# Kernel optimization log

Hardware: AMD Instinct MI355X
Metric: run time of the kernel (lower is better)

The kernel has to match this reference:

```python
import jax, jax.numpy as jnp
import numpy as np

N, E = 50000, 800000
IN_F, OUT_F, H = 128, 128, 4
D = OUT_F // H  # head dim
NEG_SLOPE = 0.2
EPS = 1e-12


def setup_inputs() -> dict:
    key = jax.random.key(0)
    ks = jax.random.split(key, 10)
    s = 1.0 / np.sqrt(IN_F)
    return {
        "x": jax.random.normal(ks[0], (N, IN_F), jnp.float32),
        "W_src": jax.random.normal(ks[1], (IN_F, H * D), jnp.float32) * s,
        "b_src": jnp.zeros((H * D,), jnp.float32),
        "W_dst": jax.random.normal(ks[2], (IN_F, H * D), jnp.float32) * s,
        "b_dst": jnp.zeros((H * D,), jnp.float32),
        "attn": jax.random.normal(ks[3], (H, D), jnp.float32) * (1.0 / np.sqrt(D)),
        "out_bias": jnp.zeros((H * D,), jnp.float32),
        "ln_w": jnp.ones((OUT_F,), jnp.float32),
        "ln_b": jnp.zeros((OUT_F,), jnp.float32),
        "src": jax.random.randint(ks[4], (E,), 0, N, jnp.int32),
        "dst": jax.random.randint(ks[5], (E,), 0, N, jnp.int32),
    }


def reference(x, W_src, b_src, W_dst, b_dst, attn, out_bias, ln_w, ln_b, src, dst):
    n = x.shape[0]
    # GATv2Conv (share_weights=False): separate source/dest projections
    fs = (x @ W_src + b_src).reshape(n, H, D)  # [N,H,D]
    fd = (x @ W_dst + b_dst).reshape(n, H, D)
    # per-edge scores: e_ij = attn . leaky_relu(fs[u] + fd[v])
    e = jax.nn.leaky_relu(fs[src] + fd[dst], NEG_SLOPE)  # [E,H,D]
    logits = jnp.einsum("ehd,hd->eh", e, attn)  # [E,H]
    # edge softmax over incoming edges of each dst node
    m = jax.ops.segment_max(logits, dst, num_segments=n)  # [N,H]
    ex = jnp.exp(logits - m[dst])
    denom = jax.ops.segment_sum(ex, dst, num_segments=n)  # [N,H]
    alpha = ex / denom[dst]  # [E,H]
    # aggregate: sum_j alpha_ij * fs[j]
    msg = alpha[:, :, None] * fs[src]  # [E,H,D]
    rst = jax.ops.segment_sum(msg, dst, num_segments=n)  # [N,H,D]
    h = rst.reshape(n, H * D) + out_bias
    # LayerNorm (biased variance, eps inside sqrt)
    u = h.mean(-1, keepdims=True)
    s = jnp.mean((h - u) ** 2, -1, keepdims=True)
    h = (h - u) / jnp.sqrt(s + EPS)
    h = ln_w * h + ln_b
    # activation = elu; dropout p=0 -> identity
    return jax.nn.elu(h)
```

## Files before the change

kernel.cpp:

```cpp
#include <hip/hip_runtime.h>
#include <hip/hip_bf16.h>

constexpr int NF = 128;

using bf16x8 = __attribute__((ext_vector_type(8))) short;
using f32x4v = __attribute__((ext_vector_type(4))) float;

__device__ __forceinline__ unsigned short f2bs(float f) {
    return __builtin_bit_cast(unsigned short, __float2bfloat16(f));
}
__device__ __forceinline__ void unpack8(float4 raw, float* a) {
    unsigned u0 = __float_as_uint(raw.x);
    unsigned u1 = __float_as_uint(raw.y);
    unsigned u2 = __float_as_uint(raw.z);
    unsigned u3 = __float_as_uint(raw.w);
    a[0] = __uint_as_float(u0 << 16);
    a[1] = __uint_as_float(u0 & 0xffff0000u);
    a[2] = __uint_as_float(u1 << 16);
    a[3] = __uint_as_float(u1 & 0xffff0000u);
    a[4] = __uint_as_float(u2 << 16);
    a[5] = __uint_as_float(u2 & 0xffff0000u);
    a[6] = __uint_as_float(u3 << 16);
    a[7] = __uint_as_float(u3 & 0xffff0000u);
}

__global__ void GraphAttnLayer_70196945486348_kernel() {}

__device__ __forceinline__ void gemm_tile(
    const float* __restrict__ x,
    const unsigned short* __restrict__ Wb2,
    const float* __restrict__ bsrc, const float* __restrict__ bdst,
    unsigned short* __restrict__ fs, float* __restrict__ fd,
    int tile, int N)
{
    __shared__ float xs[32][129];
    const int t = threadIdx.x;
    const int lane = t & 63;
    const int wave = t >> 6;
    const int m_base = tile * 32;
    if (m_base >= N) return;
    const int lm = lane & 15;
    const int kq = (lane >> 4) * 8;

    bf16x8 bfrag[4][4];
    float bias[4];
#pragma unroll
    for (int c = 0; c < 4; ++c) {
        int col = wave * 64 + c * 16 + lm;
        bias[c] = (col < 128) ? bsrc[col] : bdst[col - 128];
#pragma unroll
        for (int s = 0; s < 4; ++s)
            bfrag[c][s] = *(const bf16x8*)(Wb2 + ((size_t)((c * 4 + s) * 256 + t)) * 8);
    }

#pragma unroll
    for (int q = 0; q < 4; ++q) {
        int idx = q * 256 + t;
        int row = idx >> 5;
        int c4  = (idx & 31) * 4;
        int grow = m_base + row;
        if (grow >= N) grow = N - 1;
        float4 v = *(const float4*)(x + (size_t)grow * NF + c4);
        xs[row][c4 + 0] = v.x;
        xs[row][c4 + 1] = v.y;
        xs[row][c4 + 2] = v.z;
        xs[row][c4 + 3] = v.w;
    }
    __syncthreads();

    for (int r = 0; r < 2; ++r) {
        int m0 = m_base + r * 16;
        if (m0 >= N) break;
        bf16x8 afrag[4];
#pragma unroll
        for (int s = 0; s < 4; ++s) {
            const float* xp = &xs[r * 16 + lm][s * 32 + kq];
#pragma unroll
            for (int j = 0; j < 8; ++j)
                afrag[s][j] = (short)f2bs(xp[j]);
        }
#pragma unroll
        for (int c = 0; c < 4; ++c) {
            f32x4v acc = {0.f, 0.f, 0.f, 0.f};
#pragma unroll
            for (int s = 0; s < 4; ++s)
                acc = __builtin_amdgcn_mfma_f32_16x16x32_bf16(afrag[s], bfrag[c][s], acc, 0, 0, 0);
            int col = wave * 64 + c * 16 + lm;
            int cc = col & 127;
#pragma unroll
            for (int rr = 0; rr < 4; ++rr) {
                int rowd = m0 + (lane >> 4) * 4 + rr;
                if (rowd < N) {
                    float v = acc[rr] + bias[c];
                    if (col < 128) fs[(size_t)rowd * NF + cc] = f2bs(v);
                    else           fd[(size_t)rowd * NF + cc] = v;
                }
            }
        }
    }
}

__global__ __launch_bounds__(256) void hist_prep_kernel(
    const int* __restrict__ dst,
    int* __restrict__ cntT,
    const float* __restrict__ Wsrc, const float* __restrict__ Wdst,
    unsigned short* __restrict__ Wb2,
    int* __restrict__ state,
    int E, int C, int B, int NSB)
{
    __shared__ int lh[256];
    const int t = threadIdx.x;
    int gi = blockIdx.x * 256 + t;
    if (gi < NSB) state[gi] = 0;
    if (gi < 16 * 256) {
        int j = gi >> 8;
        int tt = gi & 255;
        int wave = tt >> 6;
        int lane = tt & 63;
        int lm = lane & 15;
        int kq = (lane >> 4) * 8;
        int c = j >> 2, s = j & 3;
        int col = wave * 64 + c * 16 + lm;
        int ks = s * 32 + kq;
        bf16x8 frag;
#pragma unroll
        for (int m = 0; m < 8; ++m) {
            float v = (col < 128) ? Wsrc[(ks + m) * NF + col]
                                  : Wdst[(ks + m) * NF + (col - 128)];
            frag[m] = (short)f2bs(v);
        }
        *(bf16x8*)(Wb2 + (size_t)gi * 8) = frag;
    }

    lh[t] = 0;
    __syncthreads();
    int e0 = blockIdx.x * 4096;
#pragma unroll
    for (int j = 0; j < 16; ++j) {
        int e = e0 + j * 256 + t;
        if (e < E) atomicAdd(&lh[dst[e] >> 8], 1);
    }
    __syncthreads();
    if (t < B) cntT[t * C + blockIdx.x] = lh[t];
}

__global__ __launch_bounds__(256) void scan_kernel(
    const int* __restrict__ cntT, int* __restrict__ baseBC,
    int* __restrict__ state, int M)
{
    int b = blockIdx.x, t = threadIdx.x;
    int i = b * 256 + t;
    int v = (i < M) ? cntT[i] : 0;

    __shared__ int arr[256];
    __shared__ int s_bofs;
    arr[t] = v;
    __syncthreads();
    for (int off = 1; off < 256; off <<= 1) {
        int u = (t >= off) ? arr[t - off] : 0;
        __syncthreads();
        arr[t] += u;
        __syncthreads();
    }
    int total = arr[255];

    if (t < 64) {
        if (t == 0) {
            int word = ((b == 0 ? 2 : 1) << 30) | total;
            atomicExch(&state[b], word);
        }
        int bofs = 0;
        if (b > 0) {
            int base = b;
            for (;;) {
                int j = base - 1 - t;
                int sv = 0, f = 1;
                if (j >= 0) {
                    sv = __hip_atomic_load(&state[j], __ATOMIC_RELAXED,
                                           __HIP_MEMORY_SCOPE_AGENT);
                    f = ((unsigned)sv) >> 30;
                }
                unsigned long long notready = __ballot(f == 0);
                if (notready) continue;
                unsigned long long has2 = __ballot(f == 2);
                if (has2) {
                    int k = (int)(__ffsll((unsigned long long)has2) - 1);
                    int val = (t <= k) ? (sv & 0x3FFFFFFF) : 0;
#pragma unroll
                    for (int off = 32; off; off >>= 1) val += __shfl_xor(val, off);
                    bofs += val;
                    break;
                } else {
                    int val = (j >= 0) ? (sv & 0x3FFFFFFF) : 0;
#pragma unroll
                    for (int off = 32; off; off >>= 1) val += __shfl_xor(val, off);
                    bofs += val;
                    base -= 64;
                }
            }
            if (t == 0) atomicExch(&state[b], (2 << 30) | (bofs + total));
        }
        if (t == 0) s_bofs = bofs;
    }
    __syncthreads();
    int excl = arr[t] - v + s_bofs;
    if (i < M) baseBC[i] = excl;
}

__global__ __launch_bounds__(256) void scatter_gemm_kernel(
    const int* __restrict__ dst, const int* __restrict__ src,
    const int* __restrict__ baseBC, unsigned* __restrict__ pairs,
    const float* __restrict__ x, const unsigned short* __restrict__ Wb2,
    const float* __restrict__ bsrc, const float* __restrict__ bdst,
    unsigned short* __restrict__ fs, float* __restrict__ fd,
    int N, int E, int C, int B)
{
    __shared__ int base_lds[256];
    __shared__ int lcnt[256];
    int t = threadIdx.x;
    if (blockIdx.x < (unsigned)C) {
        int chunk = blockIdx.x;
        if (t < B) base_lds[t] = baseBC[t * C + chunk];
        lcnt[t] = 0;
        __syncthreads();
        int e0 = chunk * 4096;
#pragma unroll
        for (int j = 0; j < 16; ++j) {
            int e = e0 + j * 256 + t;
            if (e < E) {
                int d = dst[e];
                int b = d >> 8;
                int r = atomicAdd(&lcnt[b], 1);
                pairs[base_lds[b] + r] = ((unsigned)(d & 255) << 16) | (unsigned)src[e];
            }
        }
    } else {
        gemm_tile(x, Wb2, bsrc, bdst, fs, fd, blockIdx.x - C, N);
    }
}

__global__ __launch_bounds__(256) void sort_gemm_kernel(
    const unsigned* __restrict__ pairs, const int* __restrict__ baseBC,
    int* __restrict__ rowptr, unsigned short* __restrict__ src_sorted,
    const float* __restrict__ x, const unsigned short* __restrict__ Wb2,
    const float* __restrict__ bsrc, const float* __restrict__ bdst,
    unsigned short* __restrict__ fs, float* __restrict__ fd,
    int N, int E, int C, int B, int T1)
{
    __shared__ int h[256];
    __shared__ int arr[256];
    __shared__ int cur[256];
    __shared__ unsigned short sorted[16384];
    int t = threadIdx.x;
    if (blockIdx.x < (unsigned)B) {
        int b = blockIdx.x;
        int segbase = baseBC[b * C];
        int end = (b + 1 < B) ? baseBC[(b + 1) * C] : E;
        int count = end - segbase;

        h[t] = 0;
        __syncthreads();
        for (int i = t; i < count; i += 256)
            atomicAdd(&h[pairs[segbase + i] >> 16], 1);
        __syncthreads();
        int v = h[t];
        arr[t] = v;
        __syncthreads();
        for (int off = 1; off < 256; off <<= 1) {
            int u = (t >= off) ? arr[t - off] : 0;
            __syncthreads();
            arr[t] += u;
            __syncthreads();
        }
        int excl = arr[t] - v;
        int node = b * 256 + t;
        if (node <= N) rowptr[node] = segbase + excl;
        cur[t] = excl;
        __syncthreads();
        for (int i = t; i < count; i += 256) {
            unsigned p = pairs[segbase + i];
            int r = atomicAdd(&cur[p >> 16], 1);
            sorted[r] = (unsigned short)(p & 0xFFFF);
        }
        __syncthreads();
        for (int i = t; i < count; i += 256)
            src_sorted[segbase + i] = sorted[i];
    } else {
        gemm_tile(x, Wb2, bsrc, bdst, fs, fd, T1 + (blockIdx.x - B), N);
    }
}

__global__ __launch_bounds__(256) void node_kernel(
    const float4* __restrict__ fsq,
    const int* __restrict__ rowptr, const unsigned short* __restrict__ src_sorted,
    const float4* __restrict__ attn4,
    const float4* __restrict__ obias4,
    const float4* __restrict__ lnw4,
    const float4* __restrict__ lnb4,
    float4* __restrict__ out4, int N)
{
    int lane = threadIdx.x & 63;
    int es = lane >> 4;
    int g  = lane & 15;
    int n = blockIdx.x * 4 + (threadIdx.x >> 6);
    if (n >= N) return;

    float4 fda = out4[(size_t)n * 32 + g * 2];
    float4 fdb = out4[(size_t)n * 32 + g * 2 + 1];
    float4 ava = attn4[g * 2];
    float4 avb = attn4[g * 2 + 1];
    float fd[8] = {fda.x, fda.y, fda.z, fda.w, fdb.x, fdb.y, fdb.z, fdb.w};
    float av[8] = {ava.x, ava.y, ava.z, ava.w, avb.x, avb.y, avb.z, avb.w};

    int beg = rowptr[n], end = rowptr[n + 1];
    float l = 0.f;
    float ac[8] = {0.f, 0.f, 0.f, 0.f, 0.f, 0.f, 0.f, 0.f};

    for (int j = beg; j < end; j += 4) {
        int idx = j + es;
        bool valid = idx < end;
        int s = src_sorted[valid ? idx : (end - 1)];
        float4 raw = fsq[(size_t)s * 16 + g];
        float a[8];
        unpack8(raw, a);
        float p = 0.f;
#pragma unroll
        for (int d = 0; d < 8; ++d) {
            float t = a[d] + fd[d];
            t = fmaxf(t, 0.2f * t);
            p += av[d] * t;
        }
        p += __shfl_xor(p, 1);
        p += __shfl_xor(p, 2);
        float e = valid ? __expf(p) : 0.f;
        l += e;
#pragma unroll
        for (int d = 0; d < 8; ++d) ac[d] += e * a[d];
    }

    l += __shfl_xor(l, 16);
    l += __shfl_xor(l, 32);
#pragma unroll
    for (int d = 0; d < 8; ++d) {
        ac[d] += __shfl_xor(ac[d], 16);
        ac[d] += __shfl_xor(ac[d], 32);
    }

    float rl = (l > 0.f) ? (1.f / l) : 0.f;
    float4 oba = obias4[g * 2];
    float4 obb = obias4[g * 2 + 1];
    float ob[8] = {oba.x, oba.y, oba.z, oba.w, obb.x, obb.y, obb.z, obb.w};
    float h[8];
    float s1 = 0.f, s2 = 0.f;
#pragma unroll
    for (int d = 0; d < 8; ++d) {
        h[d] = ac[d] * rl + ob[d];
        s1 += h[d];
        s2 += h[d] * h[d];
    }
    s1 += __shfl_xor(s1, 1); s2 += __shfl_xor(s2, 1);
    s1 += __shfl_xor(s1, 2); s2 += __shfl_xor(s2, 2);
    s1 += __shfl_xor(s1, 4); s2 += __shfl_xor(s2, 4);
    s1 += __shfl_xor(s1, 8); s2 += __shfl_xor(s2, 8);

    float u = s1 * (1.f / NF);
    float var = s2 * (1.f / NF) - u * u;
    float rstd = rsqrtf(fmaxf(var, 0.f) + 1e-12f);
    float4 gwa = lnw4[g * 2], gwb = lnw4[g * 2 + 1];
    float4 gba = lnb4[g * 2], gbb = lnb4[g * 2 + 1];
    float gw[8] = {gwa.x, gwa.y, gwa.z, gwa.w, gwb.x, gwb.y, gwb.z, gwb.w};
    float gb[8] = {gba.x, gba.y, gba.z, gba.w, gbb.x, gbb.y, gbb.z, gbb.w};
    float z[8];
#pragma unroll
    for (int d = 0; d < 8; ++d) {
        float y = gw[d] * ((h[d] - u) * rstd) + gb[d];
        z[d] = (y > 0.f) ? y : (__expf(y) - 1.f);
    }
    if (es == 0) {
        out4[(size_t)n * 32 + g * 2]     = make_float4(z[0], z[1], z[2], z[3]);
        out4[(size_t)n * 32 + g * 2 + 1] = make_float4(z[4], z[5], z[6], z[7]);
    }
}

extern "C" void kernel_launch(void* const* d_in, const int* in_sizes, int n_in,
                              void* d_out, int out_size, void* d_ws, size_t ws_size,
                              hipStream_t stream)
{
    const float* x    = (const float*)d_in[0];
    const float* Wsrc = (const float*)d_in[1];
    const float* bsrc = (const float*)d_in[2];
    const float* Wdst = (const float*)d_in[3];
    const float* bdst = (const float*)d_in[4];
    const float4* attn4 = (const float4*)d_in[5];
    const float4* obias4= (const float4*)d_in[6];
    const float4* lnw4  = (const float4*)d_in[7];
    const float4* lnb4  = (const float4*)d_in[8];
    const int* src = (const int*)d_in[9];
    const int* dst = (const int*)d_in[10];
    int N = in_sizes[0] / NF;
    int E = in_sizes[9];

    int C = (E + 4095) / 4096;
    int B = (N + 255) / 256;
    int M = B * C;
    int NSB = (M + 255) / 256;
    int T = (N + 31) / 32;
    int T1 = T / 2;
    int T2 = T - T1;

    int* cntT = (int*)d_ws;
    int* baseBC = cntT + M;
    int* state = baseBC + M;
    int* rowptr = state + 256;
    unsigned* pairs = (unsigned*)(rowptr + (N + 1));
    unsigned short* srcs = (unsigned short*)(pairs + E);
    unsigned short* Wb2 = srcs + ((E + 1) & ~1);
    unsigned short* fs = Wb2 + 16 * 256 * 8;

    hist_prep_kernel<<<C, 256, 0, stream>>>(dst, cntT, Wsrc, Wdst, Wb2,
                                            state, E, C, B, NSB);
    scan_kernel<<<NSB, 256, 0, stream>>>(cntT, baseBC, state, M);
    scatter_gemm_kernel<<<C + T1, 256, 0, stream>>>(
        dst, src, baseBC, pairs, x, Wb2, bsrc, bdst, fs, (float*)d_out,
        N, E, C, B);
    sort_gemm_kernel<<<B + T2, 256, 0, stream>>>(
        pairs, baseBC, rowptr, srcs, x, Wb2, bsrc, bdst, fs, (float*)d_out,
        N, E, C, B, T1);
    node_kernel<<<(N + 3) / 4, 256, 0, stream>>>(
        (const float4*)fs, rowptr, srcs, attn4, obias4, lnw4, lnb4,
        (float4*)d_out, N);
}
```

Before: 184.6 us.

## Vectorize edge loads, prefetch next gather in aggregation, rebalance GEMM split

The histogram and scatter passes now read dst/src as int4 for full 4096-edge chunks, which cuts load instruction count; partial chunks keep the old scalar path. The aggregation loop software-pipelines the fs gather by loading the next edge's row before computing the current one, so gather latency overlaps with ALU work. The GEMM tile split between the scatter and sort kernels moves from one half to five eighths in the scatter launch. Together these target memory latency and load imbalance, at the cost of more registers in the aggregation kernel and extra code paths.

```diff
diff --git a/kernel.cpp b/kernel.cpp
--- a/kernel.cpp
+++ b/kernel.cpp
@@ -135,10 +135,22 @@
     lh[t] = 0;
     __syncthreads();
     int e0 = blockIdx.x * 4096;
-#pragma unroll
-    for (int j = 0; j < 16; ++j) {
-        int e = e0 + j * 256 + t;
-        if (e < E) atomicAdd(&lh[dst[e] >> 8], 1);
+    if (e0 + 4096 <= E) {
+        const int4* dst4 = (const int4*)(dst + e0);
+#pragma unroll
+        for (int r = 0; r < 4; ++r) {
+            int4 d = dst4[r * 256 + t];
+            atomicAdd(&lh[d.x >> 8], 1);
+            atomicAdd(&lh[d.y >> 8], 1);
+            atomicAdd(&lh[d.z >> 8], 1);
+            atomicAdd(&lh[d.w >> 8], 1);
+        }
+    } else {
+#pragma unroll
+        for (int j = 0; j < 16; ++j) {
+            int e = e0 + j * 256 + t;
+            if (e < E) atomicAdd(&lh[dst[e] >> 8], 1);
+        }
     }
     __syncthreads();
     if (t < B) cntT[t * C + blockIdx.x] = lh[t];
@@ -224,14 +236,33 @@
         lcnt[t] = 0;
         __syncthreads();
         int e0 = chunk * 4096;
-#pragma unroll
-        for (int j = 0; j < 16; ++j) {
-            int e = e0 + j * 256 + t;
-            if (e < E) {
-                int d = dst[e];
-                int b = d >> 8;
-                int r = atomicAdd(&lcnt[b], 1);
-                pairs[base_lds[b] + r] = ((unsigned)(d & 255) << 16) | (unsigned)src[e];
+        if (e0 + 4096 <= E) {
+            const int4* dst4 = (const int4*)(dst + e0);
+            const int4* src4 = (const int4*)(src + e0);
+#pragma unroll
+            for (int r = 0; r < 4; ++r) {
+                int4 d = dst4[r * 256 + t];
+                int4 s = src4[r * 256 + t];
+                int b0 = d.x >> 8, b1 = d.y >> 8, b2 = d.z >> 8, b3 = d.w >> 8;
+                int r0 = atomicAdd(&lcnt[b0], 1);
+                int r1 = atomicAdd(&lcnt[b1], 1);
+                int r2 = atomicAdd(&lcnt[b2], 1);
+                int r3 = atomicAdd(&lcnt[b3], 1);
+                pairs[base_lds[b0] + r0] = ((unsigned)(d.x & 255) << 16) | (unsigned)s.x;
+                pairs[base_lds[b1] + r1] = ((unsigned)(d.y & 255) << 16) | (unsigned)s.y;
+                pairs[base_lds[b2] + r2] = ((unsigned)(d.z & 255) << 16) | (unsigned)s.z;
+                pairs[base_lds[b3] + r3] = ((unsigned)(d.w & 255) << 16) | (unsigned)s.w;
+            }
+        } else {
+#pragma unroll
+            for (int j = 0; j < 16; ++j) {
+                int e = e0 + j * 256 + t;
+                if (e < E) {
+                    int d = dst[e];
+                    int b = d >> 8;
+                    int r = atomicAdd(&lcnt[b], 1);
+                    pairs[base_lds[b] + r] = ((unsigned)(d & 255) << 16) | (unsigned)src[e];
+                }
             }
         }
     } else {
@@ -316,26 +347,42 @@
     float l = 0.f;
     float ac[8] = {0.f, 0.f, 0.f, 0.f, 0.f, 0.f, 0.f, 0.f};
 
-    for (int j = beg; j < end; j += 4) {
-        int idx = j + es;
+    if (beg < end) {
+        int idx = beg + es;
         bool valid = idx < end;
         int s = src_sorted[valid ? idx : (end - 1)];
         float4 raw = fsq[(size_t)s * 16 + g];
-        float a[8];
-        unpack8(raw, a);
-        float p = 0.f;
-#pragma unroll
-        for (int d = 0; d < 8; ++d) {
-            float t = a[d] + fd[d];
-            t = fmaxf(t, 0.2f * t);
-            p += av[d] * t;
-        }
-        p += __shfl_xor(p, 1);
-        p += __shfl_xor(p, 2);
-        float e = valid ? __expf(p) : 0.f;
-        l += e;
-#pragma unroll
-        for (int d = 0; d < 8; ++d) ac[d] += e * a[d];
+
+        for (int j = beg; j < end; j += 4) {
+            int jn = j + 4;
+            bool vn = false;
+            float4 rawn = raw;
+            if (jn < end) {
+                int idxn = jn + es;
+                vn = idxn < end;
+                int sn = src_sorted[vn ? idxn : (end - 1)];
+                rawn = fsq[(size_t)sn * 16 + g];
+            }
+
+            float a[8];
+            unpack8(raw, a);
+            float p = 0.f;
+#pragma unroll
+            for (int d = 0; d < 8; ++d) {
+                float t = a[d] + fd[d];
+                t = fmaxf(t, 0.2f * t);
+                p += av[d] * t;
+            }
+            p += __shfl_xor(p, 1);
+            p += __shfl_xor(p, 2);
+            float e = valid ? __expf(p) : 0.f;
+            l += e;
+#pragma unroll
+            for (int d = 0; d < 8; ++d) ac[d] += e * a[d];
+
+            valid = vn;
+            raw = rawn;
+        }
     }
 
     l += __shfl_xor(l, 16);
@@ -405,7 +452,7 @@
     int M = B * C;
     int NSB = (M + 255) / 256;
     int T = (N + 31) / 32;
-    int T1 = T / 2;
+    int T1 = (T * 5) / 8;
     int T2 = T - T1;
 
     int* cntT = (int*)d_ws;
```

After: 176.1 us. 1.05x faster.
